# Optimization experiments

Hardware: AMD Instinct MI355X
Metric: run time of the kernel (lower is better)

## Reference

```python
import jax, jax.numpy as jnp
import numpy as np

B, C_IN, T = 256, 7, 160
PATCH, D_MODEL, N_LAYERS = 10, 512, 2
D_STATE, D_CONV, EXPAND = 16, 4, 2
L_TOK = T // PATCH            # 16 tokens
D_INNER = EXPAND * D_MODEL    # 1024
DT_RANK = D_MODEL // 16       # 32
EPS = 1e-5


def setup_inputs() -> dict:
    key = jax.random.key(0)
    ks = iter(jax.random.split(key, 32))
    def rn(shape, s=0.02):
        return jax.random.normal(next(ks), shape, dtype=jnp.float32) * s
    return {
        'x': jax.random.normal(next(ks), (B, C_IN, T), dtype=jnp.float32),
        'bn_gamma': jnp.ones((C_IN,), jnp.float32),
        'bn_beta': jnp.zeros((C_IN,), jnp.float32),
        'bn_mean': jnp.zeros((C_IN,), jnp.float32),
        'bn_var': jnp.ones((C_IN,), jnp.float32),
        'patch_w': rn((D_MODEL, C_IN * PATCH)),
        'patch_b': jnp.zeros((D_MODEL,), jnp.float32),
        'ln_patch_g': jnp.ones((D_MODEL,), jnp.float32),
        'ln_patch_b': jnp.zeros((D_MODEL,), jnp.float32),
        'pos': rn((1, L_TOK, D_MODEL)),
        'blk_ln_g': jnp.ones((N_LAYERS, D_MODEL), jnp.float32),
        'blk_ln_b': jnp.zeros((N_LAYERS, D_MODEL), jnp.float32),
        'in_proj_w': rn((N_LAYERS, 2, D_MODEL, 2 * D_INNER)),
        'conv_w': rn((N_LAYERS, 2, D_INNER, D_CONV), 0.1),
        'conv_b': jnp.zeros((N_LAYERS, 2, D_INNER), jnp.float32),
        'x_proj_w': rn((N_LAYERS, 2, D_INNER, DT_RANK + 2 * D_STATE)),
        'dt_proj_w': rn((N_LAYERS, 2, DT_RANK, D_INNER), 0.1),
        'dt_proj_b': jnp.full((N_LAYERS, 2, D_INNER), -4.6, jnp.float32),
        'A_log': jnp.tile(jnp.log(jnp.arange(1, D_STATE + 1, dtype=jnp.float32)), (N_LAYERS, 2, D_INNER, 1)),
        'Dskip': jnp.ones((N_LAYERS, 2, D_INNER), jnp.float32),
        'out_proj_w': rn((N_LAYERS, 2, D_INNER, D_MODEL)),
        'final_ln_g': jnp.ones((D_MODEL,), jnp.float32),
        'final_ln_b': jnp.zeros((D_MODEL,), jnp.float32),
    }


def _ln(x, g, b):
    m = x.mean(-1, keepdims=True)
    v = ((x - m) ** 2).mean(-1, keepdims=True)
    return (x - m) * jax.lax.rsqrt(v + EPS) * g + b


def _mamba_dir(x, Wi, cw, cb, Wx, Wdt, bdt, A_log, Dv, Wo):
    # x: (B, L, d_model) -> (B, L, d_model); one-direction S6 mamba
    u, z = jnp.split(x @ Wi, 2, axis=-1)              # (B,L,D_INNER) each
    Lq = u.shape[1]
    up = jnp.pad(u, ((0, 0), (D_CONV - 1, 0), (0, 0)))  # causal depthwise conv
    uc = cb + sum(up[:, k:k + Lq, :] * cw[:, k] for k in range(D_CONV))
    uc = jax.nn.silu(uc)
    proj = uc @ Wx                                     # (B,L,DT_RANK+2*D_STATE)
    dtr = proj[..., :DT_RANK]
    Bm = proj[..., DT_RANK:DT_RANK + D_STATE]
    Cm = proj[..., DT_RANK + D_STATE:]
    dt = jax.nn.softplus(dtr @ Wdt + bdt)              # (B,L,D_INNER)
    A = -jnp.exp(A_log)                                # (D_INNER,D_STATE)
    dA = jnp.exp(dt[..., None] * A)                    # (B,L,D_INNER,D_STATE)
    dBu = (dt * uc)[..., None] * Bm[:, :, None, :]     # (B,L,D_INNER,D_STATE)

    def step(h, inp):
        dA_t, dBu_t, C_t = inp
        h = dA_t * h + dBu_t                           # (B,D_INNER,D_STATE)
        return h, jnp.einsum('bdn,bn->bd', h, C_t)

    h0 = jnp.zeros((x.shape[0], D_INNER, D_STATE), x.dtype)
    _, ys = jax.lax.scan(step, h0, (dA.swapaxes(0, 1), dBu.swapaxes(0, 1), Cm.swapaxes(0, 1)))
    y = ys.swapaxes(0, 1) + uc * Dv
    return (y * jax.nn.silu(z)) @ Wo


def reference(x, bn_gamma, bn_beta, bn_mean, bn_var, patch_w, patch_b,
              ln_patch_g, ln_patch_b, pos, blk_ln_g, blk_ln_b, in_proj_w,
              conv_w, conv_b, x_proj_w, dt_proj_w, dt_proj_b, A_log, Dskip,
              out_proj_w, final_ln_g, final_ln_b):
    # 1. input BatchNorm1d (eval mode, running stats)
    xn = (x - bn_mean[:, None]) * jax.lax.rsqrt(bn_var[:, None] + EPS) * bn_gamma[:, None] + bn_beta[:, None]
    # 2. patch embed: (B,C,T) -> (B,L,C*PATCH) -> (B,L,d_model)
    p = xn.reshape(B, C_IN, L_TOK, PATCH).transpose(0, 2, 1, 3).reshape(B, L_TOK, C_IN * PATCH)
    h = _ln(p @ patch_w.T + patch_b, ln_patch_g, ln_patch_b)
    # 3. positional embedding
    h = h + pos[:, :L_TOK]
    # 4. Bi-Mamba blocks
    for i in range(N_LAYERS):
        hn = _ln(h, blk_ln_g[i], blk_ln_b[i])
        yf = _mamba_dir(hn, in_proj_w[i, 0], conv_w[i, 0], conv_b[i, 0], x_proj_w[i, 0],
                        dt_proj_w[i, 0], dt_proj_b[i, 0], A_log[i, 0], Dskip[i, 0], out_proj_w[i, 0])
        yb = _mamba_dir(hn[:, ::-1], in_proj_w[i, 1], conv_w[i, 1], conv_b[i, 1], x_proj_w[i, 1],
                        dt_proj_w[i, 1], dt_proj_b[i, 1], A_log[i, 1], Dskip[i, 1], out_proj_w[i, 1])[:, ::-1]
        h = h + yf + yb
    # 5. final LayerNorm
    return _ln(h, final_ln_g, final_ln_b)
```

## Files before the change

### kernel.cpp

```cpp
#include <hip/hip_runtime.h>
#include <math.h>
#include <stdint.h>

#define BB 256
#define C_IN 7
#define TT 160
#define PATCH 10
#define D_MODEL 512
#define L_TOK 16
#define D_INNER 1024
#define D_STATE 16
#define DT_RANK 32
#define EPS 1e-5f
#define NROWS (BB*L_TOK)
#define KPAD 96

typedef __bf16 bf16x8 __attribute__((ext_vector_type(8)));
typedef __bf16 bf16x4 __attribute__((ext_vector_type(4)));
typedef float  f32x4  __attribute__((ext_vector_type(4)));

__device__ __forceinline__ float siluf(float x){ return x / (1.f + __expf(-x)); }
__device__ __forceinline__ float softplusf(float x){ return (x > 20.f) ? x : log1pf(__expf(x)); }

__device__ __forceinline__ void gload_lds16(const void* gp, void* lp){
  __builtin_amdgcn_global_load_lds(
      (const __attribute__((address_space(1))) unsigned int*)(uintptr_t)gp,
      (__attribute__((address_space(3))) unsigned int*)(uintptr_t)lp, 16, 0, 0);
}

__device__ __forceinline__ float block_reduce_sum(float v, float* sred4){
  for(int off=32; off>0; off>>=1) v += __shfl_down(v, off, 64);
  int lane = threadIdx.x & 63, wid = threadIdx.x >> 6;
  if(lane==0) sred4[wid] = v;
  __syncthreads();
  if(threadIdx.x==0) sred4[0] = sred4[0]+sred4[1]+sred4[2]+sred4[3];
  __syncthreads();
  float r = sred4[0];
  __syncthreads();
  return r;
}

__global__ __launch_bounds__(256) void transpose_bf16_kernel(
    const float* __restrict__ in, __bf16* __restrict__ out, int K, int N)
{
  __shared__ float tile[32][33];
  size_t moff = (size_t)blockIdx.z * K * N;
  int n0 = blockIdx.x*32, k0 = blockIdx.y*32;
  int tx = threadIdx.x, ty = threadIdx.y;
  #pragma unroll
  for(int rr=0;rr<4;rr++)
    tile[ty+rr*8][tx] = in[moff + (size_t)(k0+ty+rr*8)*N + n0+tx];
  __syncthreads();
  #pragma unroll
  for(int rr=0;rr<4;rr++)
    out[moff + (size_t)(n0+ty+rr*8)*K + k0+tx] = (__bf16)tile[tx][ty+rr*8];
}

__global__ __launch_bounds__(256) void transpose_outw_kernel(
    const float* __restrict__ in, __bf16* __restrict__ out)
{
  __shared__ float tile[32][33];
  int z = blockIdx.z, layer = z>>1, dir = z&1;
  int n0 = blockIdx.x*32, k0 = blockIdx.y*32;
  int tx = threadIdx.x, ty = threadIdx.y;
  const float* ip = in + (size_t)z*1024*512;
  #pragma unroll
  for(int rr=0;rr<4;rr++)
    tile[ty+rr*8][tx] = ip[(size_t)(k0+ty+rr*8)*512 + n0+tx];
  __syncthreads();
  __bf16* op = out + (size_t)layer*512*2048 + (size_t)dir*1024;
  #pragma unroll
  for(int rr=0;rr<4;rr++)
    op[(size_t)(n0+ty+rr*8)*2048 + k0+tx] = (__bf16)tile[tx][ty+rr*8];
}

__global__ __launch_bounds__(256) void bn_patchify_kernel(
    const float* __restrict__ x, const float* __restrict__ bng,
    const float* __restrict__ bnb, const float* __restrict__ bnm,
    const float* __restrict__ bnv, __bf16* __restrict__ Abuf)
{
  int idx = blockIdx.x*256 + threadIdx.x;
  int row = idx / KPAD, k = idx % KPAD;
  int b = row >> 4, l = row & 15;
  float v = 0.f;
  if(k < C_IN*PATCH){
    int c = k / PATCH, j = k % PATCH;
    float xv = x[(b*C_IN + c)*TT + l*PATCH + j];
    v = (xv - bnm[c]) * rsqrtf(bnv[c] + EPS) * bng[c] + bnb[c];
  }
  Abuf[idx] = (__bf16)v;
}

__global__ __launch_bounds__(256) void cast_pad_pw_kernel(
    const float* __restrict__ pw, __bf16* __restrict__ pwb)
{
  int idx = blockIdx.x*256 + threadIdx.x;
  if(idx >= 512*KPAD) return;
  int n = idx / KPAD, k = idx % KPAD;
  pwb[idx] = (__bf16)(k < C_IN*PATCH ? pw[n*(C_IN*PATCH) + k] : 0.f);
}

template<int BM, int BN, int BK, int ACC, int EPI>
__global__ __launch_bounds__(256) void mfma_gemm(
    const __bf16* __restrict__ A, const __bf16* __restrict__ Bt,
    float* __restrict__ C, __bf16* __restrict__ Cb,
    const float* __restrict__ bias, int N, int K, int lda, int ldb,
    size_t sA, size_t sB, size_t sC, size_t sBias)
{
  constexpr int NGA = BM/16, NGB = BN/16;
  constexpr int APW = NGA/4, BPW = NGB/4;
  constexpr int MI  = BM/32, FN  = BN/32;
  constexpr int NSL = BK/32;
  __shared__ __align__(16) __bf16 As[NSL*NGA*512];
  __shared__ __align__(16) __bf16 Bs[NSL*NGB*512];
  int z = blockIdx.z;
  A  += (size_t)z*sA;  Bt += (size_t)z*sB;
  if(EPI==0 || EPI==1) C  += (size_t)z*sC;
  if(EPI!=0)           Cb += (size_t)z*sC;
  if(EPI==2)           bias += (size_t)z*sBias;
  int tid  = threadIdx.x;
  int lane = tid & 63, w = tid >> 6;
  int wrow = w >> 1, wcol = w & 1;
  int r = lane & 15, q = lane >> 4;
  int row0 = blockIdx.y*BM, col0 = blockIdx.x*BN;

  f32x4 acc[MI][FN];
  #pragma unroll
  for(int i=0;i<MI;i++)
    #pragma unroll
    for(int j=0;j<FN;j++) acc[i][j] = (f32x4)0.f;

  const __bf16* aSrc[APW];
  #pragma unroll
  for(int g=0;g<APW;g++)
    aSrc[g] = A + (size_t)(row0 + (w*APW+g)*16 + r)*lda + q*8;
  const __bf16* bSrc[BPW];
  #pragma unroll
  for(int g=0;g<BPW;g++)
    bSrc[g] = Bt + (size_t)(col0 + (w*BPW+g)*16 + r)*ldb + q*8;

  for(int k0=0;k0<K;k0+=BK){
    #pragma unroll
    for(int s=0;s<NSL;s++){
      #pragma unroll
      for(int g=0;g<APW;g++)
        gload_lds16(aSrc[g] + k0 + s*32, As + (s*NGA + w*APW+g)*512);
      #pragma unroll
      for(int g=0;g<BPW;g++)
        gload_lds16(bSrc[g] + k0 + s*32, Bs + (s*NGB + w*BPW+g)*512);
    }
    __syncthreads();
    #pragma unroll
    for(int s=0;s<NSL;s++){
      bf16x8 aF[MI], bF[FN];
      #pragma unroll
      for(int i=0;i<MI;i++)
        aF[i] = *(const bf16x8*)(As + (s*NGA + wrow*MI+i)*512 + lane*8);
      #pragma unroll
      for(int j=0;j<FN;j++)
        bF[j] = *(const bf16x8*)(Bs + (s*NGB + wcol*FN+j)*512 + lane*8);
      #pragma unroll
      for(int i=0;i<MI;i++)
        #pragma unroll
        for(int j=0;j<FN;j++)
          acc[i][j] = __builtin_amdgcn_mfma_f32_16x16x32_bf16(bF[j], aF[i], acc[i][j], 0, 0, 0);
    }
    __syncthreads();
  }

  #pragma unroll
  for(int i=0;i<MI;i++){
    int m = row0 + wrow*(BM/2) + i*16 + r;
    #pragma unroll
    for(int j=0;j<FN;j++){
      int n = col0 + wcol*(BN/2) + j*16 + q*4;
      if(EPI==2){
        const float* bp = bias + n;
        bf16x4 hv;
        #pragma unroll
        for(int p=0;p<4;p++) hv[p] = (__bf16)softplusf(acc[i][j][p] + bp[p]);
        *(bf16x4*)(Cb + (size_t)m*N + n) = hv;
      } else if(EPI==3){
        bf16x4 hv;
        #pragma unroll
        for(int p=0;p<4;p++) hv[p] = (__bf16)acc[i][j][p];
        *(bf16x4*)(Cb + (size_t)m*N + n) = hv;
      } else {
        float* cp = C + (size_t)m*N + n;
        f32x4 ov = acc[i][j];
        if(ACC){
          f32x4 cv = *(const f32x4*)cp;
          #pragma unroll
          for(int p=0;p<4;p++) ov[p] += cv[p];
        }
        *(f32x4*)cp = ov;
        if(EPI==1){
          bf16x4 hv;
          #pragma unroll
          for(int p=0;p<4;p++) hv[p] = (__bf16)ov[p];
          *(bf16x4*)(Cb + (size_t)m*N + n) = hv;
        }
      }
    }
  }
}

__global__ __launch_bounds__(256, 3) void mfma_inproj_conv(
    const __bf16* __restrict__ A, const __bf16* __restrict__ Bt,
    const float* __restrict__ cw, const float* __restrict__ cb,
    __bf16* __restrict__ ucb, __bf16* __restrict__ szb)
{
  constexpr int LDA = 512, LDB = 512, K = 512;
  __shared__ __align__(16) __bf16 As[2*8*512];
  __shared__ __align__(16) __bf16 Bs[2*4*512];
  __shared__ float4 s_w4[64];
  __shared__ float  s_b[64];
  int tid  = threadIdx.x;
  int lane = tid & 63, w = tid >> 6;
  int wrow = w >> 1, wcol = w & 1;
  int r = lane & 15, q = lane >> 4;

  int lin  = blockIdx.x + gridDim.x*blockIdx.y;
  int xcd  = lin & 7;
  int idx  = lin >> 3;
  int colb = xcd*8 + (idx & 7);
  int rowb = idx >> 3;
  int row0 = rowb*128, col0 = colb*64;

  int dirq = col0 >> 11;
  int feat0 = col0 & 2047;
  bool is_u = feat0 < 1024;
  int dblk = col0 & 1023;
  const float* cwd = cw + dirq*4096;
  const float* cbd = cb + dirq*1024;
  if(is_u && tid < 64){
    s_w4[tid] = ((const float4*)cwd)[dblk + tid];
    s_b[tid]  = cbd[dblk + tid];
  }

  f32x4 acc[4][2];
  #pragma unroll
  for(int i=0;i<4;i++)
    #pragma unroll
    for(int j=0;j<2;j++) acc[i][j] = (f32x4)0.f;

  const __bf16* aSrc[2];
  #pragma unroll
  for(int g=0;g<2;g++)
    aSrc[g] = A + (size_t)(row0 + (w*2+g)*16 + r)*LDA + q*8;
  const __bf16* bSrc0 = Bt + (size_t)(col0 + w*16 + r)*LDB + q*8;

  for(int k0=0;k0<K;k0+=64){
    #pragma unroll
    for(int s=0;s<2;s++){
      #pragma unroll
      for(int g=0;g<2;g++)
        gload_lds16(aSrc[g] + k0 + s*32, As + (s*8 + w*2+g)*512);
      gload_lds16(bSrc0 + k0 + s*32, Bs + (s*4 + w)*512);
    }
    __syncthreads();
    #pragma unroll
    for(int s=0;s<2;s++){
      bf16x8 aF[4], bF[2];
      #pragma unroll
      for(int i=0;i<4;i++)
        aF[i] = *(const bf16x8*)(As + (s*8 + wrow*4+i)*512 + lane*8);
      #pragma unroll
      for(int j=0;j<2;j++)
        bF[j] = *(const bf16x8*)(Bs + (s*4 + wcol*2+j)*512 + lane*8);
      #pragma unroll
      for(int i=0;i<4;i++)
        #pragma unroll
        for(int j=0;j<2;j++)
          acc[i][j] = __builtin_amdgcn_mfma_f32_16x16x32_bf16(bF[j], aF[i], acc[i][j], 0, 0, 0);
    }
    __syncthreads();
  }

  __bf16* ucbD = ucb + (size_t)dirq*NROWS*1024;
  __bf16* szD  = szb + (size_t)dirq*NROWS*1024;

  #pragma unroll
  for(int i=0;i<4;i++){
    int tok = row0 + wrow*64 + i*16 + r;
    #pragma unroll
    for(int j=0;j<2;j++){
      int nloc = wcol*32 + j*16 + q*4;
      if(is_u){
        int f = nloc;
        int d = dblk + f;
        float vout[4];
        if(dirq==0){
          #pragma unroll
          for(int p=0;p<4;p++){
            float cur = acc[i][j][p];
            float m1 = __shfl_up(cur, 1, 64);
            float m2 = __shfl_up(cur, 2, 64);
            float m3 = __shfl_up(cur, 3, 64);
            float4 w4 = s_w4[f+p];
            float v = s_b[f+p] + w4.w*cur;
            v += (r>=1)? w4.z*m1 : 0.f;
            v += (r>=2)? w4.y*m2 : 0.f;
            v += (r>=3)? w4.x*m3 : 0.f;
            vout[p] = v;
          }
        } else {
          #pragma unroll
          for(int p=0;p<4;p++){
            float cur = acc[i][j][p];
            float p1 = __shfl_down(cur, 1, 64);
            float p2 = __shfl_down(cur, 2, 64);
            float p3 = __shfl_down(cur, 3, 64);
            float4 w4 = s_w4[f+p];
            float v = s_b[f+p] + w4.w*cur;
            v += (r<=14)? w4.z*p1 : 0.f;
            v += (r<=13)? w4.y*p2 : 0.f;
            v += (r<=12)? w4.x*p3 : 0.f;
            vout[p] = v;
          }
        }
        bf16x4 hv;
        #pragma unroll
        for(int p=0;p<4;p++) hv[p] = (__bf16)siluf(vout[p]);
        *(bf16x4*)(ucbD + (size_t)tok*1024 + d) = hv;
      } else {
        int dz = feat0 - 1024 + nloc;
        bf16x4 hv;
        #pragma unroll
        for(int p=0;p<4;p++) hv[p] = (__bf16)siluf(acc[i][j][p]);
        *(bf16x4*)(szD + (size_t)tok*1024 + dz) = hv;
      }
    }
  }
}

__global__ __launch_bounds__(256) void ln_pos_kernel(
    const float* __restrict__ in, const float* __restrict__ pb,
    const float* __restrict__ g, const float* __restrict__ bt,
    const float* __restrict__ pos, float* __restrict__ out)
{
  __shared__ float sred[4];
  int row = blockIdx.x; int l = row & 15; int tid = threadIdx.x;
  const float* ip = in + (size_t)row*512;
  float v0 = ip[tid] + pb[tid], v1 = ip[tid+256] + pb[tid+256];
  float s = block_reduce_sum(v0+v1, sred);
  float mean = s * (1.f/512.f);
  float d0 = v0-mean, d1 = v1-mean;
  float vs = block_reduce_sum(d0*d0+d1*d1, sred);
  float rstd = rsqrtf(vs*(1.f/512.f) + EPS);
  out[(size_t)row*512+tid]     = d0*rstd*g[tid]     + bt[tid]     + pos[l*512+tid];
  out[(size_t)row*512+tid+256] = d1*rstd*g[tid+256] + bt[tid+256] + pos[l*512+tid+256];
}

__global__ __launch_bounds__(256) void ln_bf16_kernel(
    const float* __restrict__ in, const float* __restrict__ g,
    const float* __restrict__ bt, __bf16* __restrict__ out)
{
  __shared__ float sred[4];
  int row = blockIdx.x; int tid = threadIdx.x;
  const float* ip = in + (size_t)row*512;
  float v0 = ip[tid], v1 = ip[tid+256];
  float s = block_reduce_sum(v0+v1, sred);
  float mean = s * (1.f/512.f);
  float d0 = v0-mean, d1 = v1-mean;
  float vs = block_reduce_sum(d0*d0+d1*d1, sred);
  float rstd = rsqrtf(vs*(1.f/512.f) + EPS);
  out[(size_t)row*512+tid]     = (__bf16)(d0*rstd*g[tid]     + bt[tid]);
  out[(size_t)row*512+tid+256] = (__bf16)(d1*rstd*g[tid+256] + bt[tid+256]);
}

__global__ __launch_bounds__(256) void ln_f32_kernel(
    const float* __restrict__ in, const float* __restrict__ g,
    const float* __restrict__ bt, float* __restrict__ out)
{
  __shared__ float sred[4];
  int row = blockIdx.x; int tid = threadIdx.x;
  const float* ip = in + (size_t)row*512;
  float v0 = ip[tid], v1 = ip[tid+256];
  float s = block_reduce_sum(v0+v1, sred);
  float mean = s * (1.f/512.f);
  float d0 = v0-mean, d1 = v1-mean;
  float vs = block_reduce_sum(d0*d0+d1*d1, sred);
  float rstd = rsqrtf(vs*(1.f/512.f) + EPS);
  out[(size_t)row*512+tid]     = d0*rstd*g[tid]     + bt[tid];
  out[(size_t)row*512+tid+256] = d1*rstd*g[tid+256] + bt[tid+256];
}

__global__ __launch_bounds__(256) void scan_kernel(
    const __bf16* __restrict__ dtb, const __bf16* __restrict__ ucb,
    const __bf16* __restrict__ projb, const __bf16* __restrict__ szb,
    const float* __restrict__ A_log, const float* __restrict__ Dskip,
    __bf16* __restrict__ gb)
{
  int b = blockIdx.x;
  int dirq = blockIdx.y >> 2;
  int d = (blockIdx.y & 3)*256 + threadIdx.x;
  const __bf16* dtp = dtb + (size_t)dirq*NROWS*1024;
  const __bf16* ucp = ucb + (size_t)dirq*NROWS*1024;
  const __bf16* prp = projb + (size_t)dirq*NROWS*64;
  const __bf16* szp = szb  + (size_t)dirq*NROWS*1024;
  const float*  Alp = A_log + (size_t)dirq*1024*16;
  float Dv = Dskip[dirq*1024 + d];
  __shared__ float sB[16][16], sC[16][16];
  {
    int s = threadIdx.x >> 4, n = threadIdx.x & 15;
    int tok = dirq ? 15-s : s;
    sB[s][n] = (float)prp[(size_t)(b*16+tok)*64 + 32 + n];
    sC[s][n] = (float)prp[(size_t)(b*16+tok)*64 + 48 + n];
  }
  __syncthreads();
  float a[16], hst[16];
  #pragma unroll
  for(int n=0;n<16;n++){ a[n] = -__expf(Alp[d*16+n]); hst[n]=0.f; }
  for(int s=0;s<16;s++){
    int tok = dirq ? 15-s : s;
    size_t o = (size_t)(b*16+tok)*1024 + d;
    float dtv = (float)dtp[o];
    float ucv = (float)ucp[o];
    float dtu = dtv*ucv;
    float y = 0.f;
    #pragma unroll
    for(int n=0;n<16;n++){
      hst[n] = __expf(dtv*a[n])*hst[n] + dtu*sB[s][n];
      y += hst[n]*sC[s][n];
    }
    float zs = (float)szp[o];
    gb[(size_t)(b*16+tok)*2048 + dirq*1024 + d] = (__bf16)((y + ucv*Dv) * zs);
  }
}

extern "C" void kernel_launch(void* const* d_in, const int* in_sizes, int n_in,
                              void* d_out, int out_size, void* d_ws, size_t ws_size,
                              hipStream_t stream) {
  (void)in_sizes; (void)n_in; (void)out_size; (void)ws_size;
  const float* x         = (const float*)d_in[0];
  const float* bn_gamma  = (const float*)d_in[1];
  const float* bn_beta   = (const float*)d_in[2];
  const float* bn_mean   = (const float*)d_in[3];
  const float* bn_var    = (const float*)d_in[4];
  const float* patch_w   = (const float*)d_in[5];
  const float* patch_b   = (const float*)d_in[6];
  const float* ln_pg     = (const float*)d_in[7];
  const float* ln_pb     = (const float*)d_in[8];
  const float* pos       = (const float*)d_in[9];
  const float* blk_ln_g  = (const float*)d_in[10];
  const float* blk_ln_b  = (const float*)d_in[11];
  const float* in_proj_w = (const float*)d_in[12];
  const float* conv_w    = (const float*)d_in[13];
  const float* conv_b    = (const float*)d_in[14];
  const float* x_proj_w  = (const float*)d_in[15];
  const float* dt_proj_w = (const float*)d_in[16];
  const float* dt_proj_b = (const float*)d_in[17];
  const float* A_log     = (const float*)d_in[18];
  const float* Dskip     = (const float*)d_in[19];
  const float* out_proj_w= (const float*)d_in[20];
  const float* fin_g     = (const float*)d_in[21];
  const float* fin_b     = (const float*)d_in[22];

  char* p = (char*)d_ws;
  float*  h    = (float*)p;  p += (size_t)NROWS*512*4;
  __bf16* hnb  = (__bf16*)p; p += (size_t)NROWS*512*2;
  __bf16* ucb2 = (__bf16*)p; p += (size_t)2*NROWS*1024*2;
  __bf16* szb2 = (__bf16*)p; p += (size_t)2*NROWS*1024*2;
  __bf16* dtb2 = (__bf16*)p; p += (size_t)2*NROWS*1024*2;
  __bf16* gbK  = (__bf16*)p; p += (size_t)NROWS*2048*2;
  __bf16* projb2=(__bf16*)p; p += (size_t)2*NROWS*64*2;
  __bf16* wtin = (__bf16*)p; p += (size_t)4*2048*512*2;
  __bf16* wtoutK=(__bf16*)p; p += (size_t)2*512*2048*2;
  __bf16* wtx  = (__bf16*)p; p += (size_t)4*64*1024*2;
  __bf16* wdtT = (__bf16*)p; p += (size_t)4*1024*32*2;
  __bf16* Abuf = (__bf16*)p; p += (size_t)NROWS*KPAD*2;
  __bf16* pwb  = (__bf16*)p; p += (size_t)512*KPAD*2;

  transpose_bf16_kernel<<<dim3(64, 16, 4), dim3(32,8), 0, stream>>>(
      in_proj_w, wtin, 512, 2048);
  transpose_outw_kernel<<<dim3(16, 32, 4), dim3(32,8), 0, stream>>>(
      out_proj_w, wtoutK);
  transpose_bf16_kernel<<<dim3(2, 32, 4), dim3(32,8), 0, stream>>>(
      x_proj_w, wtx, 1024, 64);
  transpose_bf16_kernel<<<dim3(32, 1, 4), dim3(32,8), 0, stream>>>(
      dt_proj_w, wdtT, 32, 1024);
  cast_pad_pw_kernel<<<(512*KPAD + 255)/256, 256, 0, stream>>>(patch_w, pwb);

  bn_patchify_kernel<<<(NROWS*KPAD)/256, 256, 0, stream>>>(
      x, bn_gamma, bn_beta, bn_mean, bn_var, Abuf);
  mfma_gemm<128,128,32,0,0><<<dim3(4, 32, 1), 256, 0, stream>>>(
      Abuf, pwb, (float*)gbK, nullptr, nullptr, 512, KPAD, KPAD, KPAD, 0,0,0,0);
  ln_pos_kernel<<<NROWS, 256, 0, stream>>>((float*)gbK, patch_b, ln_pg, ln_pb, pos, h);

  for(int i=0;i<2;i++){
    ln_bf16_kernel<<<NROWS, 256, 0, stream>>>(h, blk_ln_g + i*512, blk_ln_b + i*512, hnb);
    mfma_inproj_conv<<<dim3(64, 32), 256, 0, stream>>>(
        hnb, wtin + (size_t)i*4096*512, conv_w + (size_t)i*2*4096,
        conv_b + (size_t)i*2*1024, ucb2, szb2);
    mfma_gemm<64,64,64,0,3><<<dim3(1, 64, 2), 256, 0, stream>>>(
        ucb2, wtx + (size_t)i*2*64*1024, nullptr, projb2, nullptr,
        64, 1024, 1024, 1024,
        (size_t)NROWS*1024, (size_t)64*1024, (size_t)NROWS*64, 0);
    mfma_gemm<64,64,32,0,2><<<dim3(16, 64, 2), 256, 0, stream>>>(
        projb2, wdtT + (size_t)i*2*1024*32, nullptr, dtb2, dt_proj_b + (size_t)i*2*1024,
        1024, 32, 64, 32,
        (size_t)NROWS*64, (size_t)1024*32, (size_t)NROWS*1024, 1024);
    scan_kernel<<<dim3(BB, 8), 256, 0, stream>>>(
        dtb2, ucb2, projb2, szb2, A_log + (size_t)i*2*1024*16,
        Dskip + (size_t)i*2*1024, gbK);
    mfma_gemm<64,64,64,1,0><<<dim3(8, 64, 1), 256, 0, stream>>>(
        gbK, wtoutK + (size_t)i*512*2048, h, nullptr, nullptr,
        512, 2048, 2048, 2048, 0,0,0,0);
  }
  ln_f32_kernel<<<NROWS, 256, 0, stream>>>(h, fin_g, fin_b, (float*)d_out);
}
```

Baseline: 492.0 us.

## Stage full weight tile in LDS, stream activations from global into registers

The in-projection+conv GEMM kernel now loads the block's entire 64xK weight slice into shared memory once, instead of double-buffering A and B tiles per k-step with two barriers each iteration. Each warp owns 32 rows and all 64 columns, reading its A fragments directly from global memory into registers with one-step software prefetch. This removes per-iteration __syncthreads and A staging through LDS. In exchange LDS use grows to 64KB per block, occupancy drops (the launch bound of 3 blocks was removed), and A is loaded from global memory by each wave without sharing.

```diff
diff --git a/kernel.cpp b/kernel.cpp
--- a/kernel.cpp
+++ b/kernel.cpp
@@ -205,19 +205,17 @@
   }
 }
 
-__global__ __launch_bounds__(256, 3) void mfma_inproj_conv(
+__global__ __launch_bounds__(256) void mfma_inproj_conv(
     const __bf16* __restrict__ A, const __bf16* __restrict__ Bt,
     const float* __restrict__ cw, const float* __restrict__ cb,
     __bf16* __restrict__ ucb, __bf16* __restrict__ szb)
 {
-  constexpr int LDA = 512, LDB = 512, K = 512;
-  __shared__ __align__(16) __bf16 As[2*8*512];
-  __shared__ __align__(16) __bf16 Bs[2*4*512];
+  constexpr int K = 512;
+  __shared__ __align__(16) __bf16 Bs[16*4*512];
   __shared__ float4 s_w4[64];
   __shared__ float  s_b[64];
   int tid  = threadIdx.x;
   int lane = tid & 63, w = tid >> 6;
-  int wrow = w >> 1, wcol = w & 1;
   int r = lane & 15, q = lane >> 4;
 
   int lin  = blockIdx.x + gridDim.x*blockIdx.y;
@@ -231,61 +229,63 @@
   int feat0 = col0 & 2047;
   bool is_u = feat0 < 1024;
   int dblk = col0 & 1023;
-  const float* cwd = cw + dirq*4096;
-  const float* cbd = cb + dirq*1024;
   if(is_u && tid < 64){
-    s_w4[tid] = ((const float4*)cwd)[dblk + tid];
-    s_b[tid]  = cbd[dblk + tid];
-  }
-
-  f32x4 acc[4][2];
-  #pragma unroll
-  for(int i=0;i<4;i++)
-    #pragma unroll
-    for(int j=0;j<2;j++) acc[i][j] = (f32x4)0.f;
-
-  const __bf16* aSrc[2];
-  #pragma unroll
-  for(int g=0;g<2;g++)
-    aSrc[g] = A + (size_t)(row0 + (w*2+g)*16 + r)*LDA + q*8;
-  const __bf16* bSrc0 = Bt + (size_t)(col0 + w*16 + r)*LDB + q*8;
-
-  for(int k0=0;k0<K;k0+=64){
-    #pragma unroll
-    for(int s=0;s<2;s++){
-      #pragma unroll
-      for(int g=0;g<2;g++)
-        gload_lds16(aSrc[g] + k0 + s*32, As + (s*8 + w*2+g)*512);
-      gload_lds16(bSrc0 + k0 + s*32, Bs + (s*4 + w)*512);
+    s_w4[tid] = ((const float4*)(cw + dirq*4096))[dblk + tid];
+    s_b[tid]  = (cb + dirq*1024)[dblk + tid];
+  }
+
+  {
+    const __bf16* bSrc = Bt + (size_t)(col0 + w*16 + r)*K + q*8;
+    #pragma unroll
+    for(int s=0;s<16;s++)
+      gload_lds16(bSrc + s*32, Bs + (s*4 + w)*512);
+  }
+
+  f32x4 acc[2][4];
+  #pragma unroll
+  for(int i=0;i<2;i++)
+    #pragma unroll
+    for(int j=0;j<4;j++) acc[i][j] = (f32x4)0.f;
+
+  const __bf16* aPtr[2];
+  #pragma unroll
+  for(int i=0;i<2;i++)
+    aPtr[i] = A + (size_t)(row0 + w*32 + i*16 + r)*K + q*8;
+
+  bf16x8 aCur[2], aNxt[2];
+  #pragma unroll
+  for(int i=0;i<2;i++) aCur[i] = *(const bf16x8*)(aPtr[i]);
+
+  __syncthreads();
+
+  #pragma unroll
+  for(int s=0;s<16;s++){
+    if(s<15){
+      #pragma unroll
+      for(int i=0;i<2;i++) aNxt[i] = *(const bf16x8*)(aPtr[i] + (s+1)*32);
     }
-    __syncthreads();
-    #pragma unroll
-    for(int s=0;s<2;s++){
-      bf16x8 aF[4], bF[2];
-      #pragma unroll
-      for(int i=0;i<4;i++)
-        aF[i] = *(const bf16x8*)(As + (s*8 + wrow*4+i)*512 + lane*8);
-      #pragma unroll
-      for(int j=0;j<2;j++)
-        bF[j] = *(const bf16x8*)(Bs + (s*4 + wcol*2+j)*512 + lane*8);
-      #pragma unroll
-      for(int i=0;i<4;i++)
-        #pragma unroll
-        for(int j=0;j<2;j++)
-          acc[i][j] = __builtin_amdgcn_mfma_f32_16x16x32_bf16(bF[j], aF[i], acc[i][j], 0, 0, 0);
-    }
-    __syncthreads();
+    bf16x8 bF[4];
+    #pragma unroll
+    for(int j=0;j<4;j++)
+      bF[j] = *(const bf16x8*)(Bs + (s*4 + j)*512 + lane*8);
+    #pragma unroll
+    for(int i=0;i<2;i++)
+      #pragma unroll
+      for(int j=0;j<4;j++)
+        acc[i][j] = __builtin_amdgcn_mfma_f32_16x16x32_bf16(bF[j], aCur[i], acc[i][j], 0, 0, 0);
+    #pragma unroll
+    for(int i=0;i<2;i++) aCur[i] = aNxt[i];
   }
 
   __bf16* ucbD = ucb + (size_t)dirq*NROWS*1024;
   __bf16* szD  = szb + (size_t)dirq*NROWS*1024;
 
   #pragma unroll
-  for(int i=0;i<4;i++){
-    int tok = row0 + wrow*64 + i*16 + r;
-    #pragma unroll
-    for(int j=0;j<2;j++){
-      int nloc = wcol*32 + j*16 + q*4;
+  for(int i=0;i<2;i++){
+    int tok = row0 + w*32 + i*16 + r;
+    #pragma unroll
+    for(int j=0;j<4;j++){
+      int nloc = j*16 + q*4;
       if(is_u){
         int f = nloc;
         int d = dblk + f;
```

New measurement: 510.5 us. +3.8%, slower.

## Split-K the x_proj and out_proj GEMMs to raise block parallelism

Applied to the files above, without the earlier changes.

The x_proj GEMM, which had only 128 blocks, is split four ways along K per direction into fp32 partial buffers, and a new reduce kernel sums the partials and casts them to bf16. The out_proj GEMM is split four ways along K and accumulates into the residual h with fp32 atomicAdd instead of a read-modify-write. Both changes aim to fill more CUs on small-N GEMMs. The cost is extra launches, partial-buffer traffic, atomic contention, and a non-deterministic summation order.

```diff
diff --git a/kernel.cpp b/kernel.cpp
--- a/kernel.cpp
+++ b/kernel.cpp
@@ -98,6 +98,17 @@
   if(idx >= 512*KPAD) return;
   int n = idx / KPAD, k = idx % KPAD;
   pwb[idx] = (__bf16)(k < C_IN*PATCH ? pw[n*(C_IN*PATCH) + k] : 0.f);
+}
+
+__global__ __launch_bounds__(256) void reduce_proj_kernel(
+    const float* __restrict__ part, __bf16* __restrict__ projb)
+{
+  int idx = blockIdx.x*256 + threadIdx.x;
+  int dir = idx / (NROWS*64);
+  int rem = idx - dir*(NROWS*64);
+  const float* p0 = part + (size_t)dir*4*NROWS*64 + rem;
+  float s = p0[0] + p0[(size_t)NROWS*64] + p0[(size_t)2*NROWS*64] + p0[(size_t)3*NROWS*64];
+  projb[idx] = (__bf16)s;
 }
 
 template<int BM, int BN, int BK, int ACC, int EPI>
@@ -187,18 +198,23 @@
         *(bf16x4*)(Cb + (size_t)m*N + n) = hv;
       } else {
         float* cp = C + (size_t)m*N + n;
-        f32x4 ov = acc[i][j];
-        if(ACC){
-          f32x4 cv = *(const f32x4*)cp;
+        if(ACC==2){
           #pragma unroll
-          for(int p=0;p<4;p++) ov[p] += cv[p];
-        }
-        *(f32x4*)cp = ov;
-        if(EPI==1){
-          bf16x4 hv;
-          #pragma unroll
-          for(int p=0;p<4;p++) hv[p] = (__bf16)ov[p];
-          *(bf16x4*)(Cb + (size_t)m*N + n) = hv;
+          for(int p=0;p<4;p++) atomicAdd(cp + p, acc[i][j][p]);
+        } else {
+          f32x4 ov = acc[i][j];
+          if(ACC==1){
+            f32x4 cv = *(const f32x4*)cp;
+            #pragma unroll
+            for(int p=0;p<4;p++) ov[p] += cv[p];
+          }
+          *(f32x4*)cp = ov;
+          if(EPI==1){
+            bf16x4 hv;
+            #pragma unroll
+            for(int p=0;p<4;p++) hv[p] = (__bf16)ov[p];
+            *(bf16x4*)(Cb + (size_t)m*N + n) = hv;
+          }
         }
       }
     }
@@ -231,11 +247,9 @@
   int feat0 = col0 & 2047;
   bool is_u = feat0 < 1024;
   int dblk = col0 & 1023;
-  const float* cwd = cw + dirq*4096;
-  const float* cbd = cb + dirq*1024;
   if(is_u && tid < 64){
-    s_w4[tid] = ((const float4*)cwd)[dblk + tid];
-    s_b[tid]  = cbd[dblk + tid];
+    s_w4[tid] = ((const float4*)(cw + dirq*4096))[dblk + tid];
+    s_b[tid]  = (cb + dirq*1024)[dblk + tid];
   }
 
   f32x4 acc[4][2];
@@ -458,19 +472,20 @@
   const float* fin_b     = (const float*)d_in[22];
 
   char* p = (char*)d_ws;
-  float*  h    = (float*)p;  p += (size_t)NROWS*512*4;
-  __bf16* hnb  = (__bf16*)p; p += (size_t)NROWS*512*2;
-  __bf16* ucb2 = (__bf16*)p; p += (size_t)2*NROWS*1024*2;
-  __bf16* szb2 = (__bf16*)p; p += (size_t)2*NROWS*1024*2;
-  __bf16* dtb2 = (__bf16*)p; p += (size_t)2*NROWS*1024*2;
-  __bf16* gbK  = (__bf16*)p; p += (size_t)NROWS*2048*2;
-  __bf16* projb2=(__bf16*)p; p += (size_t)2*NROWS*64*2;
-  __bf16* wtin = (__bf16*)p; p += (size_t)4*2048*512*2;
-  __bf16* wtoutK=(__bf16*)p; p += (size_t)2*512*2048*2;
-  __bf16* wtx  = (__bf16*)p; p += (size_t)4*64*1024*2;
-  __bf16* wdtT = (__bf16*)p; p += (size_t)4*1024*32*2;
-  __bf16* Abuf = (__bf16*)p; p += (size_t)NROWS*KPAD*2;
-  __bf16* pwb  = (__bf16*)p; p += (size_t)512*KPAD*2;
+  float*  h     = (float*)p;  p += (size_t)NROWS*512*4;
+  float*  projP = (float*)p;  p += (size_t)2*4*NROWS*64*4;
+  __bf16* hnb   = (__bf16*)p; p += (size_t)NROWS*512*2;
+  __bf16* ucb2  = (__bf16*)p; p += (size_t)2*NROWS*1024*2;
+  __bf16* szb2  = (__bf16*)p; p += (size_t)2*NROWS*1024*2;
+  __bf16* dtb2  = (__bf16*)p; p += (size_t)2*NROWS*1024*2;
+  __bf16* gbK   = (__bf16*)p; p += (size_t)NROWS*2048*2;
+  __bf16* projb2=(__bf16*)p;  p += (size_t)2*NROWS*64*2;
+  __bf16* wtin  = (__bf16*)p; p += (size_t)4*2048*512*2;
+  __bf16* wtoutK=(__bf16*)p;  p += (size_t)2*512*2048*2;
+  __bf16* wtx   = (__bf16*)p; p += (size_t)4*64*1024*2;
+  __bf16* wdtT  = (__bf16*)p; p += (size_t)4*1024*32*2;
+  __bf16* Abuf  = (__bf16*)p; p += (size_t)NROWS*KPAD*2;
+  __bf16* pwb   = (__bf16*)p; p += (size_t)512*KPAD*2;
 
   transpose_bf16_kernel<<<dim3(64, 16, 4), dim3(32,8), 0, stream>>>(
       in_proj_w, wtin, 512, 2048);
@@ -493,10 +508,15 @@
     mfma_inproj_conv<<<dim3(64, 32), 256, 0, stream>>>(
         hnb, wtin + (size_t)i*4096*512, conv_w + (size_t)i*2*4096,
         conv_b + (size_t)i*2*1024, ucb2, szb2);
-    mfma_gemm<64,64,64,0,3><<<dim3(1, 64, 2), 256, 0, stream>>>(
-        ucb2, wtx + (size_t)i*2*64*1024, nullptr, projb2, nullptr,
-        64, 1024, 1024, 1024,
-        (size_t)NROWS*1024, (size_t)64*1024, (size_t)NROWS*64, 0);
+    for(int dir=0;dir<2;dir++){
+      mfma_gemm<64,64,64,0,0><<<dim3(1, 64, 4), 256, 0, stream>>>(
+          ucb2 + (size_t)dir*NROWS*1024,
+          wtx + (size_t)(i*2+dir)*64*1024,
+          projP + (size_t)dir*4*NROWS*64, nullptr, nullptr,
+          64, 256, 1024, 1024,
+          256, 256, (size_t)NROWS*64, 0);
+    }
+    reduce_proj_kernel<<<(2*NROWS*64)/256, 256, 0, stream>>>(projP, projb2);
     mfma_gemm<64,64,32,0,2><<<dim3(16, 64, 2), 256, 0, stream>>>(
         projb2, wdtT + (size_t)i*2*1024*32, nullptr, dtb2, dt_proj_b + (size_t)i*2*1024,
         1024, 32, 64, 32,
@@ -504,9 +524,10 @@
     scan_kernel<<<dim3(BB, 8), 256, 0, stream>>>(
         dtb2, ucb2, projb2, szb2, A_log + (size_t)i*2*1024*16,
         Dskip + (size_t)i*2*1024, gbK);
-    mfma_gemm<64,64,64,1,0><<<dim3(8, 64, 1), 256, 0, stream>>>(
+    mfma_gemm<64,64,64,2,0><<<dim3(8, 64, 4), 256, 0, stream>>>(
         gbK, wtoutK + (size_t)i*512*2048, h, nullptr, nullptr,
-        512, 2048, 2048, 2048, 0,0,0,0);
+        512, 512, 2048, 2048,
+        512, 512, 0, 0);
   }
   ln_f32_kernel<<<NROWS, 256, 0, stream>>>(h, fin_g, fin_b, (float*)d_out);
 }
```

Result: slower. 656.5 us (+33.4%).
